# Kernel tuning notes

Measured on AMD Instinct MI355X. Metric: run time of the kernel, lower is better.

## Reference

```python
import jax, jax.numpy as jnp
import numpy as np

GROUP = 64  # group_size from module


def setup_inputs() -> dict:
    key = jax.random.key(0)
    ks = jax.random.split(key, 7)
    B, S, N, K = 4, 2048, 4096, 4096  # in_features=N, out_features=K
    G = N // GROUP
    x = jax.random.normal(ks[0], (B, S, N), dtype=jnp.float32)
    W_q = jax.random.randint(ks[1], (K, N), 0, 16, dtype=jnp.int32)  # 4-bit codes
    scales = jax.random.uniform(ks[2], (K, G), dtype=jnp.float32, minval=0.01, maxval=1.0)
    zeros = jax.random.uniform(ks[3], (K, G), dtype=jnp.float32, minval=0.0, maxval=15.0)
    mask = jax.random.randint(ks[4], (K, N), 0, 2, dtype=jnp.int32)  # unstructured sparsity mask
    scale2 = jax.random.uniform(ks[5], (K, 1), dtype=jnp.float32, minval=0.5, maxval=1.5)
    bias = jax.random.normal(ks[6], (K,), dtype=jnp.float32)
    return {"x": x, "W_q": W_q, "scales": scales, "zeros": zeros,
            "mask": mask, "scale2": scale2, "bias": bias}


def _dequantize_sparse_sinq(W_q, scales, zeros, mask, scale2, dtype):
    # W_q: (K, N) int codes; scales/zeros: (K, N//GROUP) per-(row,group);
    # scale2: (K, 1) second (Sinkhorn) row scale; mask: (K, N) sparsity mask.
    K, N = W_q.shape
    G = N // GROUP
    Wg = W_q.astype(dtype).reshape(K, G, GROUP)
    W = (Wg - zeros[:, :, None]) * scales[:, :, None]  # grouped affine dequant
    W = W.reshape(K, N) * scale2                       # dual-scale compensation
    W = W * mask.astype(dtype)                         # apply unstructured sparsity
    return W


def reference(x, W_q, scales, zeros, mask, scale2, bias):
    W = _dequantize_sparse_sinq(W_q, scales, zeros, mask, scale2, x.dtype)  # (K, N)
    out = jnp.einsum('bsn,kn->bsk', x, W) + bias  # x @ W.T + bias
    return out
```

## Files before the change

### kernel.cpp

```cpp
#include <hip/hip_runtime.h>


#define M_DIM 8192
#define N_DIM 4096
#define K_DIM 4096
#define NT 64

typedef __bf16 bf16;
typedef __attribute__((ext_vector_type(8))) bf16 bf16x8;
typedef __attribute__((ext_vector_type(4))) float f32x4;
typedef __attribute__((ext_vector_type(4))) float f32x4v;
typedef __attribute__((ext_vector_type(4))) int   i32x4v;

__global__ __launch_bounds__(256) void cvt_x_kernel(const float* __restrict__ x,
                                                    bf16* __restrict__ xb) {
  const long total = (long)M_DIM * N_DIM / 8;
  const long stride = (long)gridDim.x * blockDim.x;
  for (long t = (long)blockIdx.x * blockDim.x + threadIdx.x; t < total; t += stride) {
    const long e = t * 8;
    const f32x4v v0 = __builtin_nontemporal_load(reinterpret_cast<const f32x4v*>(x + e));
    const f32x4v v1 = __builtin_nontemporal_load(reinterpret_cast<const f32x4v*>(x + e + 4));
    bf16x8 o;
    o[0] = (bf16)v0[0]; o[1] = (bf16)v0[1]; o[2] = (bf16)v0[2]; o[3] = (bf16)v0[3];
    o[4] = (bf16)v1[0]; o[5] = (bf16)v1[1]; o[6] = (bf16)v1[2]; o[7] = (bf16)v1[3];
    *reinterpret_cast<bf16x8*>(xb + e) = o;
  }
}

__global__ __launch_bounds__(256) void deq_w_kernel(const int* __restrict__ Wq,
                                                    const float* __restrict__ scales,
                                                    const float* __restrict__ zeros,
                                                    const int* __restrict__ mask,
                                                    const float* __restrict__ scale2,
                                                    bf16* __restrict__ wb) {
  const int total = K_DIM * (N_DIM / 8);
  const int stride = gridDim.x * blockDim.x;
  for (int t = blockIdx.x * blockDim.x + threadIdx.x; t < total; t += stride) {
    const int k = t >> 9;
    const int n0 = (t & 511) << 3;
    const int g = n0 >> 6;
    const float s = scales[(k << 6) + g] * scale2[k];
    const float z = zeros[(k << 6) + g];
    const long base = (long)k * N_DIM + n0;
    const i32x4v q0 = __builtin_nontemporal_load(reinterpret_cast<const i32x4v*>(Wq + base));
    const i32x4v q1 = __builtin_nontemporal_load(reinterpret_cast<const i32x4v*>(Wq + base + 4));
    const i32x4v m0 = __builtin_nontemporal_load(reinterpret_cast<const i32x4v*>(mask + base));
    const i32x4v m1 = __builtin_nontemporal_load(reinterpret_cast<const i32x4v*>(mask + base + 4));
    bf16x8 o;
    o[0] = (bf16)(((float)q0[0] - z) * s * (float)m0[0]);
    o[1] = (bf16)(((float)q0[1] - z) * s * (float)m0[1]);
    o[2] = (bf16)(((float)q0[2] - z) * s * (float)m0[2]);
    o[3] = (bf16)(((float)q0[3] - z) * s * (float)m0[3]);
    o[4] = (bf16)(((float)q1[0] - z) * s * (float)m1[0]);
    o[5] = (bf16)(((float)q1[1] - z) * s * (float)m1[1]);
    o[6] = (bf16)(((float)q1[2] - z) * s * (float)m1[2]);
    o[7] = (bf16)(((float)q1[3] - z) * s * (float)m1[3]);
    *reinterpret_cast<bf16x8*>(wb + base) = o;
  }
}

__device__ inline void gload16(const bf16* g, bf16* l) {
  __builtin_amdgcn_global_load_lds(
      (const __attribute__((address_space(1))) void*)g,
      (__attribute__((address_space(3))) void*)l, 16, 0, 0);
}

#define BARRIER asm volatile("s_barrier" ::: "memory")
#define LGKM0   asm volatile("s_waitcnt lgkmcnt(0)" ::: "memory")
#define VM6     asm volatile("s_waitcnt vmcnt(6)" ::: "memory")
#define VM0     asm volatile("s_waitcnt vmcnt(0)" ::: "memory")
#define SBAR    __builtin_amdgcn_sched_barrier(0)

__global__ __launch_bounds__(512, 2) void gemm_kernel(const bf16* __restrict__ xb,
                                                      const bf16* __restrict__ wb,
                                                      const float* __restrict__ bias,
                                                      float* __restrict__ out) {
  __shared__ bf16 lds[65536];

  const int tid = threadIdx.x;
  const int lane = tid & 63;
  const int w = tid >> 6;
  const int wr = w >> 2;
  const int wc = w & 3;

  const int gid = blockIdx.x;
  const int idx = gid >> 3;
  const int bm = (gid & 7) * 4 + (idx >> 4);
  const int bk = idx & 15;
  const long m0 = (long)bm * 256;
  const long k0 = (long)bk * 256;

  const int browA = tid >> 3;
  const int slotA = (tid & 7) ^ (browA & 7);
  const bf16* baseA = xb + (m0 + browA) * N_DIM + slotA * 8;
  const int u = tid & 255;
  const int wcb = tid >> 8;
  const int browB = u >> 3;
  const int slotB = (u & 7) ^ (browB & 7);
  const bf16* baseB = wb + (k0 + wcb * 64 + browB) * N_DIM + slotB * 8;

  const int ln15 = lane & 15;
  const int x0 = (lane >> 4) ^ (lane & 7);
  int aoffk[2], boffk[2];
#pragma unroll
  for (int kk = 0; kk < 2; ++kk) {
    const int x = x0 ^ (kk << 2);
    aoffk[kk] = (wr * 128 + ln15) * 64 + x * 8;
    boffk[kk] = 16384 + (wc * 64 + ln15) * 64 + x * 8;
  }

  f32x4 acc[8][4] = {};
  bf16x8 af[4][2], bfA[2][2], bfB[2][2];

  auto STA = [&](int tt, int bsel, int h) {
    const bf16* s = baseA + (long)(h * 64) * N_DIM + tt * 64;
    bf16* d = lds + bsel * 32768 + h * 4096 + (tid << 3);
    gload16(s, d);
    gload16(s + (long)128 * N_DIM, d + 8192);
  };
  auto STB = [&](int tt, int bsel, int h) {
    const bf16* s = baseB + (long)(h * 32) * N_DIM + tt * 64;
    bf16* d = lds + bsel * 32768 + 16384 + wcb * 4096 + h * 2048 + (u << 3);
    gload16(s, d);
    gload16(s + (long)128 * N_DIM, d + 8192);
  };
  auto LDA = [&](int cb, int mh) {
#pragma unroll
    for (int mf = 0; mf < 4; ++mf)
#pragma unroll
      for (int kk = 0; kk < 2; ++kk)
        af[mf][kk] = *reinterpret_cast<const bf16x8*>(
            lds + cb + aoffk[kk] + mh * 4096 + mf * 1024);
  };
  auto LDB = [&](bf16x8 (*bf)[2], int cb, int nh) {
#pragma unroll
    for (int nf = 0; nf < 2; ++nf)
#pragma unroll
      for (int kk = 0; kk < 2; ++kk)
        bf[nf][kk] = *reinterpret_cast<const bf16x8*>(
            lds + cb + boffk[kk] + nh * 2048 + nf * 1024);
  };
  auto MFMA_Q = [&](bf16x8 (*bf)[2], int mh, int nh) {
    __builtin_amdgcn_s_setprio(1);
#pragma unroll
    for (int kk = 0; kk < 2; ++kk)
#pragma unroll
      for (int mf = 0; mf < 4; ++mf)
#pragma unroll
        for (int nf = 0; nf < 2; ++nf)
          acc[mh * 4 + mf][nh * 2 + nf] = __builtin_amdgcn_mfma_f32_16x16x32_bf16(
              af[mf][kk], bf[nf][kk], acc[mh * 4 + mf][nh * 2 + nf], 0, 0, 0);
    __builtin_amdgcn_s_setprio(0);
  };

  STA(0, 0, 0); STB(0, 0, 0); STB(0, 0, 1); STA(0, 0, 1);
  STA(1, 1, 0); STB(1, 1, 0); STB(1, 1, 1);
  VM6; BARRIER;

  auto TILE = [&](int t, int c) {
    const int cb = c * 32768;
    LDA(cb, 0); LDB(bfA, cb, 0);
    if (t + 1 < NT) STA(t + 1, c ^ 1, 1);
    asm volatile("s_waitcnt lgkmcnt(8)" ::: "memory");
    BARRIER; LGKM0; SBAR;
    MFMA_Q(bfA, 0, 0); SBAR; BARRIER;
    LDB(bfB, cb, 1);
    if (t + 2 < NT) STA(t + 2, c, 0);
    BARRIER; LGKM0; SBAR;
    MFMA_Q(bfB, 0, 1); SBAR; BARRIER;
    LDA(cb, 1);
    if (t + 2 < NT) STB(t + 2, c, 0);
    BARRIER; LGKM0; SBAR;
    MFMA_Q(bfA, 1, 0); SBAR; BARRIER;
    if (t + 2 < NT) STB(t + 2, c, 1);
    if (t < NT - 2) { VM6; } else { VM0; }
    BARRIER; LGKM0; SBAR;
    MFMA_Q(bfB, 1, 1); SBAR; BARRIER;
  };

  for (int tp = 0; tp < NT / 2; ++tp) {
    TILE(2 * tp, 0);
    TILE(2 * tp + 1, 1);
  }

  const int ocol0 = (int)k0 + wc * 64 + ln15;
  const int orow0 = (int)m0 + wr * 128 + (lane >> 4) * 4;
#pragma unroll
  for (int ni = 0; ni < 4; ++ni) {
    const float bv = bias[ocol0 + ni * 16];
#pragma unroll
    for (int mi = 0; mi < 8; ++mi)
#pragma unroll
      for (int r = 0; r < 4; ++r)
        __builtin_nontemporal_store(
            acc[mi][ni][r] + bv,
            &out[(long)(orow0 + mi * 16 + r) * K_DIM + ocol0 + ni * 16]);
  }
}

extern "C" void kernel_launch(void* const* d_in, const int* in_sizes, int n_in,
                              void* d_out, int out_size, void* d_ws, size_t ws_size,
                              hipStream_t stream) {
  const float* x      = (const float*)d_in[0];
  const int*   Wq     = (const int*)d_in[1];
  const float* scales = (const float*)d_in[2];
  const float* zeros  = (const float*)d_in[3];
  const int*   mask   = (const int*)d_in[4];
  const float* scale2 = (const float*)d_in[5];
  const float* bias   = (const float*)d_in[6];
  float* out = (float*)d_out;

  bf16* xb = (bf16*)d_ws;
  bf16* wb = (bf16*)((char*)d_ws + (size_t)M_DIM * N_DIM * 2);

  cvt_x_kernel<<<2048, 256, 0, stream>>>(x, xb);
  deq_w_kernel<<<2048, 256, 0, stream>>>(Wq, scales, zeros, mask, scale2, wb);

  gemm_kernel<<<512, 512, 0, stream>>>(xb, wb, bias, out);
}
```

Measured before the change: 287.1 us.

## Software-pipeline LDS fragment reads under MFMA with double-buffered A fragments

Splits the A fragment registers into two halves and issues the LDS reads for the next quarter (and for the next tile's first quarter) inside the same scheduling region as the current MFMA block, so LDS latency overlaps matrix math instead of being waited on before each MFMA quarter. The first A/B fragments are preloaded before the loop. This adds register pressure (extra 8 bf16x8 fragments) under launch bounds of 512 threads with 2 blocks, and relies on the existing barriers to keep the cross-buffer prefetch of the next tile safe.

Result: no change. 287.0 us (-0.0%).

```diff
diff --git a/kernel.cpp b/kernel.cpp
--- a/kernel.cpp
+++ b/kernel.cpp
@@ -110,7 +110,7 @@
   }
 
   f32x4 acc[8][4] = {};
-  bf16x8 af[4][2], bfA[2][2], bfB[2][2];
+  bf16x8 afH0[4][2], afH1[4][2], bfA[2][2], bfB[2][2];
 
   auto STA = [&](int tt, int bsel, int h) {
     const bf16* s = baseA + (long)(h * 64) * N_DIM + tt * 64;
@@ -124,24 +124,23 @@
     gload16(s, d);
     gload16(s + (long)128 * N_DIM, d + 8192);
   };
-  auto LDA = [&](int cb, int mh) {
+  auto LDA = [&](bf16x8 (*dst)[2], int cb, int mh) {
 #pragma unroll
     for (int mf = 0; mf < 4; ++mf)
 #pragma unroll
       for (int kk = 0; kk < 2; ++kk)
-        af[mf][kk] = *reinterpret_cast<const bf16x8*>(
+        dst[mf][kk] = *reinterpret_cast<const bf16x8*>(
             lds + cb + aoffk[kk] + mh * 4096 + mf * 1024);
   };
-  auto LDB = [&](bf16x8 (*bf)[2], int cb, int nh) {
+  auto LDB = [&](bf16x8 (*dst)[2], int cb, int nh) {
 #pragma unroll
     for (int nf = 0; nf < 2; ++nf)
 #pragma unroll
       for (int kk = 0; kk < 2; ++kk)
-        bf[nf][kk] = *reinterpret_cast<const bf16x8*>(
+        dst[nf][kk] = *reinterpret_cast<const bf16x8*>(
             lds + cb + boffk[kk] + nh * 2048 + nf * 1024);
   };
-  auto MFMA_Q = [&](bf16x8 (*bf)[2], int mh, int nh) {
-    __builtin_amdgcn_s_setprio(1);
+  auto MFMA_Q = [&](bf16x8 (*a4)[2], bf16x8 (*bf)[2], int mh, int nh) {
 #pragma unroll
     for (int kk = 0; kk < 2; ++kk)
 #pragma unroll
@@ -149,33 +148,45 @@
 #pragma unroll
         for (int nf = 0; nf < 2; ++nf)
           acc[mh * 4 + mf][nh * 2 + nf] = __builtin_amdgcn_mfma_f32_16x16x32_bf16(
-              af[mf][kk], bf[nf][kk], acc[mh * 4 + mf][nh * 2 + nf], 0, 0, 0);
-    __builtin_amdgcn_s_setprio(0);
+              a4[mf][kk], bf[nf][kk], acc[mh * 4 + mf][nh * 2 + nf], 0, 0, 0);
   };
 
   STA(0, 0, 0); STB(0, 0, 0); STB(0, 0, 1); STA(0, 0, 1);
   STA(1, 1, 0); STB(1, 1, 0); STB(1, 1, 1);
   VM6; BARRIER;
+  LDA(afH0, 0, 0); LDB(bfA, 0, 0);
 
   auto TILE = [&](int t, int c) {
     const int cb = c * 32768;
-    LDA(cb, 0); LDB(bfA, cb, 0);
+    const int nb_ = (c ^ 1) * 32768;
     if (t + 1 < NT) STA(t + 1, c ^ 1, 1);
-    asm volatile("s_waitcnt lgkmcnt(8)" ::: "memory");
-    BARRIER; LGKM0; SBAR;
-    MFMA_Q(bfA, 0, 0); SBAR; BARRIER;
+    BARRIER; LGKM0; SBAR;
+    __builtin_amdgcn_s_setprio(1);
     LDB(bfB, cb, 1);
+    MFMA_Q(afH0, bfA, 0, 0);
+    __builtin_amdgcn_s_setprio(0);
+    SBAR; BARRIER;
     if (t + 2 < NT) STA(t + 2, c, 0);
     BARRIER; LGKM0; SBAR;
-    MFMA_Q(bfB, 0, 1); SBAR; BARRIER;
-    LDA(cb, 1);
+    __builtin_amdgcn_s_setprio(1);
+    LDA(afH1, cb, 1);
+    MFMA_Q(afH0, bfB, 0, 1);
+    __builtin_amdgcn_s_setprio(0);
+    SBAR; BARRIER;
     if (t + 2 < NT) STB(t + 2, c, 0);
     BARRIER; LGKM0; SBAR;
-    MFMA_Q(bfA, 1, 0); SBAR; BARRIER;
+    __builtin_amdgcn_s_setprio(1);
+    MFMA_Q(afH1, bfA, 1, 0);
+    __builtin_amdgcn_s_setprio(0);
+    SBAR; BARRIER;
     if (t + 2 < NT) STB(t + 2, c, 1);
     if (t < NT - 2) { VM6; } else { VM0; }
     BARRIER; LGKM0; SBAR;
-    MFMA_Q(bfB, 1, 1); SBAR; BARRIER;
+    __builtin_amdgcn_s_setprio(1);
+    if (t + 1 < NT) { LDA(afH0, nb_, 0); LDB(bfA, nb_, 0); }
+    MFMA_Q(afH1, bfB, 1, 1);
+    __builtin_amdgcn_s_setprio(0);
+    SBAR; BARRIER;
   };
 
   for (int tp = 0; tp < NT / 2; ++tp) {
```
